# Kernel tuning notes

Hardware: AMD Instinct MI355X
Metric: run time of the kernel (lower is better)

## Reference

```python
import jax, jax.numpy as jnp
import numpy as np

B, T, C, H = 2, 2048, 1024, 16
HD = C // H          # head dim = 64
HD2 = HD // 2        # rotary half = 32


def setup_inputs() -> dict:
    key = jax.random.key(0)
    k0, k1, k2 = jax.random.split(key, 3)
    x = jax.random.normal(k0, (B, T, C), jnp.float32)
    Wqkv = jax.random.normal(k1, (C, 3 * C), jnp.float32) * (1.0 / np.sqrt(C))
    bqkv = jnp.zeros((3 * C,), jnp.float32)
    Wproj = jax.random.normal(k2, (C, C), jnp.float32) * (1.0 / np.sqrt(C))
    bproj = jnp.zeros((C,), jnp.float32)
    # standard rotary frequencies: theta_i = 10000^{-2i/hd}
    inv_freq = 1.0 / (10000.0 ** (jnp.arange(0, HD, 2, dtype=jnp.float32) / HD))
    angles = jnp.arange(T, dtype=jnp.float32)[:, None] * inv_freq[None, :]  # (T, HD2)
    return {
        "x": x,
        "freqs_cos": jnp.cos(angles),
        "freqs_sin": jnp.sin(angles),
        "Wqkv": Wqkv,
        "bqkv": bqkv,
        "Wproj": Wproj,
        "bproj": bproj,
    }


def _rope(u, cos, sin):
    # u: (B, T, H, HD); half-split pairing: (u[i], u[i + HD/2]) form a complex pair
    u1, u2 = u[..., :HD2], u[..., HD2:]
    c = cos[None, :, None, :]  # (1, T, 1, HD2)
    s = sin[None, :, None, :]
    return jnp.concatenate([u1 * c - u2 * s, u1 * s + u2 * c], axis=-1)


def reference(x, freqs_cos, freqs_sin, Wqkv, bqkv, Wproj, bproj):
    Bc, Tc, Cc = x.shape
    qkv = x @ Wqkv + bqkv                      # (B, T, 3C)
    q, k, v = jnp.split(qkv, 3, axis=-1)
    q = q.reshape(Bc, Tc, H, HD)
    k = k.reshape(Bc, Tc, H, HD)
    v = v.reshape(Bc, Tc, H, HD)
    q = _rope(q, freqs_cos, freqs_sin)
    k = _rope(k, freqs_cos, freqs_sin)
    scale = 1.0 / np.sqrt(HD)
    scores = jnp.einsum("bthd,bshd->bhts", q, k) * scale  # (B, H, T, T)
    causal = jnp.tril(jnp.ones((Tc, Tc), dtype=bool))
    scores = jnp.where(causal[None, None], scores, jnp.finfo(scores.dtype).min)
    p = jax.nn.softmax(scores, axis=-1)
    y = jnp.einsum("bhts,bshd->bthd", p, v).reshape(Bc, Tc, Cc)
    return y @ Wproj + bproj
```

## Files before the change

kernel.cpp:

```cpp
#include <hip/hip_runtime.h>
#include <hip/hip_bf16.h>
#include <cstdint>
#include <cmath>

typedef __bf16 bf16_t;
typedef __attribute__((ext_vector_type(8))) __bf16 bf16x8;
typedef __attribute__((ext_vector_type(4))) float f32x4;

#define LOG2E 1.4426950408889634f

constexpr int B_ = 2, T_ = 2048, C_ = 1024, H_ = 16, HD_ = 64, HD2_ = 32;
constexpr int M_ = B_ * T_;

static __device__ __forceinline__ f32x4 mfma16(bf16x8 a, bf16x8 b, f32x4 c) {
    return __builtin_amdgcn_mfma_f32_16x16x32_bf16(a, b, c, 0, 0, 0);
}

#define GLL(gp, lp)                                                          \
    __builtin_amdgcn_global_load_lds(                                        \
        (const __attribute__((address_space(1))) void*)(gp),                 \
        (__attribute__((address_space(3))) void*)(lp), 16, 0, 0)

__global__ void prep(const float* __restrict__ x, bf16_t* __restrict__ xb,
                     const float* __restrict__ Wqkv, bf16_t* __restrict__ wqkvT,
                     const float* __restrict__ Wproj, bf16_t* __restrict__ wprojT) {
    __shared__ float tile[32][33];
    const int bid = blockIdx.x, tid = threadIdx.x;
    if (bid < 4096) {
        int i = bid * 256 + tid;
        float4 v = ((const float4*)x)[i];
        bf16_t o[4] = {(bf16_t)v.x, (bf16_t)v.y, (bf16_t)v.z, (bf16_t)v.w};
        *(uint64_t*)(xb + (size_t)i * 4) = *(uint64_t*)o;
        return;
    }
    const float* W;
    bf16_t* WT;
    int K, N, nb, kb;
    if (bid < 4096 + 3072) {
        int t = bid - 4096;
        W = Wqkv; WT = wqkvT; K = C_; N = 3 * C_;
        nb = (t % 96) * 32; kb = (t / 96) * 32;
    } else {
        int t = bid - 7168;
        W = Wproj; WT = wprojT; K = C_; N = C_;
        nb = (t & 31) * 32; kb = (t >> 5) * 32;
    }
    int tx = tid & 31, ty = tid >> 5;
    for (int i = ty; i < 32; i += 8)
        tile[i][tx] = W[(size_t)(kb + i) * N + nb + tx];
    __syncthreads();
    for (int i = ty; i < 32; i += 8)
        WT[(size_t)(nb + i) * K + kb + tx] = (bf16_t)tile[tx][i];
}

template <int MODE>
__global__ __launch_bounds__(256, 3) void gemm128(
    const bf16_t* __restrict__ A, const bf16_t* __restrict__ BT, const float* __restrict__ bias,
    int N, int K,
    bf16_t* __restrict__ Qb, bf16_t* __restrict__ Kb, bf16_t* __restrict__ VTb,
    const float* __restrict__ cosT, const float* __restrict__ sinT, float* __restrict__ out) {
    constexpr int NT = (MODE == 1) ? 2 : 4;
    constexpr int BPARTS = (MODE == 1) ? 2 : 4;
    __shared__ alignas(16) bf16_t As[128 * 64];
    __shared__ alignas(16) bf16_t Bs[32 * BPARTS * 64];
    const int tid = threadIdx.x;
    const int w = tid >> 6, lane = tid & 63;
    const int quad = lane >> 4, r = lane & 15;
    const int wm = (w >> 1) * 64, wn = (w & 1) * (16 * NT);
    const int bid = blockIdx.x;
    const int xcd = bid & 7, s = bid >> 3;
    int mb, nb;
    if (MODE == 0) {
        mb = (((xcd >> 1) << 3) + (s & 7)) << 7;
        nb = (((xcd & 1) * 12 + (s >> 3))) << 7;
    } else {
        mb = (((xcd >> 1) << 3) + (s & 7)) << 7;
        nb = (((xcd & 1) << 3) + (s >> 3)) << 6;
    }
    const int srow = tid >> 3, schunk = tid & 7;
    const int csw = (schunk ^ (srow & 7)) * 8;
    const int koff0 = (quad ^ (r & 7)) * 8;
    const int koff1 = ((quad + 4) ^ (r & 7)) * 8;

    f32x4 acc[4][NT] = {};

    const bf16_t* gA[4];
    const bf16_t* gB[BPARTS];
#pragma unroll
    for (int p = 0; p < 4; p++) gA[p] = A + (size_t)(mb + p * 32 + srow) * K + csw;
#pragma unroll
    for (int p = 0; p < BPARTS; p++) gB[p] = BT + (size_t)(nb + p * 32 + srow) * K + csw;

    for (int k0 = 0; k0 < K; k0 += 64) {
        __syncthreads();
#pragma unroll
        for (int p = 0; p < 4; p++) GLL(gA[p] + k0, As + p * 2048 + tid * 8);
#pragma unroll
        for (int p = 0; p < BPARTS; p++) GLL(gB[p] + k0, Bs + p * 2048 + tid * 8);
        __syncthreads();
#pragma unroll
        for (int h = 0; h < 2; h++) {
            const int ko = h ? koff1 : koff0;
            bf16x8 af[4], bfr[NT];
#pragma unroll
            for (int i = 0; i < 4; i++) af[i] = *(const bf16x8*)(As + (wm + i * 16 + r) * 64 + ko);
#pragma unroll
            for (int j = 0; j < NT; j++) bfr[j] = *(const bf16x8*)(Bs + (wn + j * 16 + r) * 64 + ko);
#pragma unroll
            for (int i = 0; i < 4; i++)
#pragma unroll
                for (int j = 0; j < NT; j++) acc[i][j] = mfma16(af[i], bfr[j], acc[i][j]);
        }
    }

    if (MODE == 0) {
        const int col_base = nb + wn;
        const int region = col_base >> 10;
        const int h = (col_base & 1023) >> 6;
        const float qscale = 0.125f * LOG2E;
        if (region < 2) {
#pragma unroll
            for (int i = 0; i < 4; i++) {
#pragma unroll
                for (int g = 0; g < 4; g++) {
                    int m = mb + wm + i * 16 + quad * 4 + g;
                    int b = m >> 11, t = m & (T_ - 1);
                    bf16_t* dst = (region == 0 ? Qb : Kb) + ((size_t)((b * H_ + h) * T_ + t)) * 64;
                    int tw = t & 7;
#pragma unroll
                    for (int j = 0; j < 2; j++) {
                        int d = j * 16 + r;
                        float u1 = acc[i][j][g] + bias[col_base + d];
                        float u2 = acc[i][j + 2][g] + bias[col_base + d + 32];
                        float c = cosT[t * HD2_ + d], s2 = sinT[t * HD2_ + d];
                        float o1 = u1 * c - u2 * s2;
                        float o2 = u1 * s2 + u2 * c;
                        if (region == 0) {
                            dst[d] = (bf16_t)(o1 * qscale);
                            dst[d + 32] = (bf16_t)(o2 * qscale);
                        } else {
                            dst[((((d >> 3) ^ tw)) << 3) | (d & 7)] = (bf16_t)o1;
                            dst[(((((d + 32) >> 3) ^ tw)) << 3) | (d & 7)] = (bf16_t)o2;
                        }
                    }
                }
            }
        } else {
#pragma unroll
            for (int i = 0; i < 4; i++) {
                int m0 = mb + wm + i * 16 + quad * 4;
                int b = m0 >> 11, t0 = m0 & (T_ - 1);
                bf16_t* base = VTb + (size_t)(b * H_ + h) * 64 * T_;
#pragma unroll
                for (int j = 0; j < 4; j++) {
                    int d = j * 16 + r;
                    float bb = bias[col_base + d];
                    bf16_t pk[4];
#pragma unroll
                    for (int g = 0; g < 4; g++) pk[g] = (bf16_t)(acc[i][j][g] + bb);
                    int c = (((t0 >> 3) & 7) ^ (d & 7));
                    int tsw = (t0 & ~63) | (c << 3) | (t0 & 7);
                    *(uint64_t*)(base + (size_t)d * T_ + tsw) = *(uint64_t*)pk;
                }
            }
        }
    } else {
#pragma unroll
        for (int i = 0; i < 4; i++)
#pragma unroll
            for (int g = 0; g < 4; g++) {
                int m = mb + wm + i * 16 + quad * 4 + g;
#pragma unroll
                for (int j = 0; j < NT; j++) {
                    int col = nb + wn + j * 16 + r;
                    out[(size_t)m * N + col] = acc[i][j][g] + bias[col];
                }
            }
    }
}

__global__ __launch_bounds__(512, 4) void attn64(
    const bf16_t* __restrict__ Qb, const bf16_t* __restrict__ Kb,
    const bf16_t* __restrict__ VTb, bf16_t* __restrict__ att) {
    __shared__ alignas(16) bf16_t Ks[2][2][4096];
    __shared__ alignas(16) bf16_t Vs[2][2][4096];
    __shared__ alignas(16) bf16_t Ps[8][1024];
    const int tid = threadIdx.x;
    const int w = tid >> 6, lane = tid & 63;
    const int grp = w >> 2, wq = w & 3;
    const int quad = lane >> 4, r = lane & 15;
    const int id = blockIdx.x;
    const int t = 31 - (id >> 5);
    const int bh = id & 31;
    const int ntiles = t + 1, nstages = (t + 2) >> 1;
    const size_t kbase = (size_t)bh * T_ * 64;
    const size_t vbase = (size_t)bh * 64 * T_;
    bf16_t* Pw = &Ps[w][0];
    const int srow = tid >> 3, schunk = tid & 7;
    const int koff0 = ((quad ^ (r & 7)) * 8);
    const int koff1 = (((quad + 4) ^ (r & 7)) * 8);

    const int qrow = t * 64 + wq * 16 + r;
    bf16x8 qf0 = *(const bf16x8*)(Qb + kbase + (size_t)qrow * 64 + quad * 8);
    bf16x8 qf1 = *(const bf16x8*)(Qb + kbase + (size_t)qrow * 64 + 32 + quad * 8);

    f32x4 oacc[4] = {};
    float l = 0.f;

    {
        const bf16_t* kg = Kb + kbase + (size_t)srow * 64 + schunk * 8;
        GLL(kg, &Ks[0][0][0] + tid * 8);
        const bf16_t* vg = VTb + vbase + (size_t)srow * T_ + schunk * 8;
        GLL(vg, &Vs[0][0][0] + tid * 8);
        if (1 < ntiles) {
            GLL(kg + 64 * 64, &Ks[0][1][0] + tid * 8);
            GLL(vg + 64, &Vs[0][1][0] + tid * 8);
        }
    }
    for (int s = 0; s < nstages; s++) {
        const int cur = s & 1;
        __syncthreads();
        if (s + 1 < nstages) {
            const int ja = 2 * (s + 1);
            const bf16_t* kg = Kb + kbase + (size_t)(ja * 64 + srow) * 64 + schunk * 8;
            const bf16_t* vg = VTb + vbase + (size_t)srow * T_ + ja * 64 + schunk * 8;
            GLL(kg, &Ks[cur ^ 1][0][0] + tid * 8);
            GLL(vg, &Vs[cur ^ 1][0][0] + tid * 8);
            if (ja + 1 < ntiles) {
                GLL(kg + 64 * 64, &Ks[cur ^ 1][1][0] + tid * 8);
                GLL(vg + 64, &Vs[cur ^ 1][1][0] + tid * 8);
            }
        }
        const int jt = 2 * s + grp;
        if (jt < ntiles) {
            const bf16_t* Kt = &Ks[cur][grp][0];
            const bf16_t* Vt = &Vs[cur][grp][0];
            f32x4 sc[4];
#pragma unroll
            for (int m0 = 0; m0 < 4; m0++) {
                const bf16_t* kp = Kt + (m0 * 16 + r) * 64;
                bf16x8 kf0 = *(const bf16x8*)(kp + koff0);
                bf16x8 kf1 = *(const bf16x8*)(kp + koff1);
                f32x4 z = {0.f, 0.f, 0.f, 0.f};
                z = mfma16(kf0, qf0, z);
                z = mfma16(kf1, qf1, z);
                sc[m0] = z;
            }
            if (jt == t) {
                const int j0 = jt * 64;
#pragma unroll
                for (int m0 = 0; m0 < 4; m0++) {
                    int kvb = j0 + m0 * 16 + quad * 4;
#pragma unroll
                    for (int g = 0; g < 4; g++)
                        if (kvb + g > qrow) sc[m0][g] = -INFINITY;
                }
            }
            float rs = 0.f;
#pragma unroll
            for (int m0 = 0; m0 < 4; m0++)
#pragma unroll
                for (int g = 0; g < 4; g++) {
                    float pp = __builtin_amdgcn_exp2f(sc[m0][g]);
                    sc[m0][g] = pp;
                    rs += pp;
                }
            l += rs;
#pragma unroll
            for (int m0 = 0; m0 < 4; m0++) {
                bf16_t hq[4];
#pragma unroll
                for (int g = 0; g < 4; g++) hq[g] = (bf16_t)sc[m0][g];
                int elem = (m0 >> 1) * 512 + (((m0 & 1) * 2 + (quad >> 1)) * 16 + r) * 8 + (quad & 1) * 4;
                *(uint64_t*)(Pw + elem) = *(uint64_t*)hq;
            }
            __builtin_amdgcn_wave_barrier();
            bf16x8 pf0 = *(const bf16x8*)(Pw + lane * 8);
            bf16x8 pf1 = *(const bf16x8*)(Pw + 512 + lane * 8);
#pragma unroll
            for (int d0 = 0; d0 < 4; d0++) {
                const bf16_t* vp = Vt + (d0 * 16 + r) * 64;
                bf16x8 vf0 = *(const bf16x8*)(vp + koff0);
                bf16x8 vf1 = *(const bf16x8*)(vp + koff1);
                oacc[d0] = mfma16(vf0, pf0, oacc[d0]);
                oacc[d0] = mfma16(vf1, pf1, oacc[d0]);
            }
        }
    }
    l += __shfl_xor(l, 16);
    l += __shfl_xor(l, 32);
    __syncthreads();
    float* Co = (float*)&Ks[0][0][0];
    float* Cl = (float*)&Vs[0][0][0];
    if (grp == 1) {
#pragma unroll
        for (int d0 = 0; d0 < 4; d0++)
            *(f32x4*)(Co + wq * 1024 + r * 64 + d0 * 16 + quad * 4) = oacc[d0];
        if (quad == 0) Cl[wq * 16 + r] = l;
    }
    __syncthreads();
    if (grp == 0) {
        float inv = 1.f / (l + Cl[wq * 16 + r]);
        const int b = bh >> 4, h = bh & 15;
        bf16_t* dst = att + ((size_t)(b * T_ + qrow)) * 1024 + h * 64;
#pragma unroll
        for (int d0 = 0; d0 < 4; d0++) {
            f32x4 o1 = *(const f32x4*)(Co + wq * 1024 + r * 64 + d0 * 16 + quad * 4);
            bf16_t hh[4];
#pragma unroll
            for (int g = 0; g < 4; g++)
                hh[g] = (bf16_t)((oacc[d0][g] + o1[g]) * inv);
            *(uint64_t*)(dst + d0 * 16 + quad * 4) = *(uint64_t*)hh;
        }
    }
}

extern "C" void kernel_launch(void* const* d_in, const int* in_sizes, int n_in,
                              void* d_out, int out_size, void* d_ws, size_t ws_size,
                              hipStream_t stream) {
    const float* x = (const float*)d_in[0];
    const float* fcos = (const float*)d_in[1];
    const float* fsin = (const float*)d_in[2];
    const float* Wqkv = (const float*)d_in[3];
    const float* bqkv = (const float*)d_in[4];
    const float* Wproj = (const float*)d_in[5];
    const float* bproj = (const float*)d_in[6];
    float* out = (float*)d_out;

    uint8_t* p = (uint8_t*)d_ws;
    size_t need = 0;
    auto take = [&](size_t bytes) {
        void* q = p;
        size_t pad = (bytes + 255) & ~(size_t)255;
        p += pad;
        need += pad;
        return q;
    };
    bf16_t* xb = (bf16_t*)take((size_t)M_ * C_ * 2);
    bf16_t* wqkvT = (bf16_t*)take((size_t)3 * C_ * C_ * 2);
    bf16_t* wprojT = (bf16_t*)take((size_t)C_ * C_ * 2);
    bf16_t* Qb = (bf16_t*)take((size_t)B_ * H_ * T_ * 64 * 2);
    bf16_t* Kb = (bf16_t*)take((size_t)B_ * H_ * T_ * 64 * 2);
    bf16_t* VTb = (bf16_t*)take((size_t)B_ * H_ * 64 * T_ * 2);
    bf16_t* attb = (bf16_t*)take((size_t)M_ * C_ * 2);
    if (ws_size < need) return;

    prep<<<8192, 256, 0, stream>>>(x, xb, Wqkv, wqkvT, Wproj, wprojT);

    gemm128<0><<<dim3(768), 256, 0, stream>>>(
        xb, wqkvT, bqkv, 3 * C_, C_, Qb, Kb, VTb, fcos, fsin, nullptr);

    attn64<<<dim3(1024), 512, 0, stream>>>(Qb, Kb, VTb, attb);

    gemm128<1><<<dim3(512), 256, 0, stream>>>(
        attb, wprojT, bproj, C_, C_, nullptr, nullptr, nullptr, nullptr, nullptr, out);
}
```

Before: 174.8 us.

## Load V fragments directly to registers and vectorize weight transpose prep

The attention kernel no longer stages V tiles through shared memory. Each wave loads its V fragments straight from global memory into registers at the start of each stage, while K double-buffering stays in LDS with clamped tile indices. This cuts LDS use, which allows a higher occupancy hint (launch_bounds 6), at the cost of less-coalesced global V reads whose latency has to be hidden behind the QK computation. The prep kernel is also vectorized: 8 elements per thread for the x cast, and 64x32 transpose tiles with 16-byte bf16 stores, halving the block count.

```diff
diff --git a/kernel.cpp b/kernel.cpp
--- a/kernel.cpp
+++ b/kernel.cpp
@@ -24,33 +24,48 @@
 __global__ void prep(const float* __restrict__ x, bf16_t* __restrict__ xb,
                      const float* __restrict__ Wqkv, bf16_t* __restrict__ wqkvT,
                      const float* __restrict__ Wproj, bf16_t* __restrict__ wprojT) {
-    __shared__ float tile[32][33];
     const int bid = blockIdx.x, tid = threadIdx.x;
-    if (bid < 4096) {
-        int i = bid * 256 + tid;
-        float4 v = ((const float4*)x)[i];
-        bf16_t o[4] = {(bf16_t)v.x, (bf16_t)v.y, (bf16_t)v.z, (bf16_t)v.w};
-        *(uint64_t*)(xb + (size_t)i * 4) = *(uint64_t*)o;
+    if (bid < 2048) {
+        size_t i = ((size_t)bid * 256 + tid) * 8;
+        float4 v0 = *(const float4*)(x + i);
+        float4 v1 = *(const float4*)(x + i + 4);
+        union { bf16_t h[8]; uint4 u; } pk;
+        pk.h[0] = (bf16_t)v0.x; pk.h[1] = (bf16_t)v0.y;
+        pk.h[2] = (bf16_t)v0.z; pk.h[3] = (bf16_t)v0.w;
+        pk.h[4] = (bf16_t)v1.x; pk.h[5] = (bf16_t)v1.y;
+        pk.h[6] = (bf16_t)v1.z; pk.h[7] = (bf16_t)v1.w;
+        *(uint4*)(xb + i) = pk.u;
         return;
     }
+    __shared__ float tile[32][66];
     const float* W;
     bf16_t* WT;
-    int K, N, nb, kb;
-    if (bid < 4096 + 3072) {
-        int t = bid - 4096;
-        W = Wqkv; WT = wqkvT; K = C_; N = 3 * C_;
-        nb = (t % 96) * 32; kb = (t / 96) * 32;
+    int N, nb, kb;
+    if (bid < 3584) {
+        int t = bid - 2048;
+        W = Wqkv; WT = wqkvT; N = 3 * C_;
+        nb = (t % 48) * 64; kb = (t / 48) * 32;
     } else {
-        int t = bid - 7168;
-        W = Wproj; WT = wprojT; K = C_; N = C_;
-        nb = (t & 31) * 32; kb = (t >> 5) * 32;
-    }
-    int tx = tid & 31, ty = tid >> 5;
-    for (int i = ty; i < 32; i += 8)
-        tile[i][tx] = W[(size_t)(kb + i) * N + nb + tx];
+        int t = bid - 3584;
+        W = Wproj; WT = wprojT; N = C_;
+        nb = (t & 15) * 64; kb = (t >> 4) * 32;
+    }
+    const int row = tid >> 3, colg = (tid & 7) * 8;
+    {
+        const float* src = W + (size_t)(kb + row) * N + nb + colg;
+        float4 a = *(const float4*)src;
+        float4 b = *(const float4*)(src + 4);
+        *(float2*)&tile[row][colg] = make_float2(a.x, a.y);
+        *(float2*)&tile[row][colg + 2] = make_float2(a.z, a.w);
+        *(float2*)&tile[row][colg + 4] = make_float2(b.x, b.y);
+        *(float2*)&tile[row][colg + 6] = make_float2(b.z, b.w);
+    }
     __syncthreads();
-    for (int i = ty; i < 32; i += 8)
-        WT[(size_t)(nb + i) * K + kb + tx] = (bf16_t)tile[tx][i];
+    const int n = tid >> 2, kg = (tid & 3) * 8;
+    union { bf16_t h[8]; uint4 u; } pk;
+#pragma unroll
+    for (int j = 0; j < 8; j++) pk.h[j] = (bf16_t)tile[kg + j][n];
+    *(uint4*)(WT + (size_t)(nb + n) * C_ + kb + kg) = pk.u;
 }
 
 template <int MODE>
@@ -179,11 +194,10 @@
     }
 }
 
-__global__ __launch_bounds__(512, 4) void attn64(
+__global__ __launch_bounds__(512, 6) void attn64(
     const bf16_t* __restrict__ Qb, const bf16_t* __restrict__ Kb,
     const bf16_t* __restrict__ VTb, bf16_t* __restrict__ att) {
     __shared__ alignas(16) bf16_t Ks[2][2][4096];
-    __shared__ alignas(16) bf16_t Vs[2][2][4096];
     __shared__ alignas(16) bf16_t Ps[8][1024];
     const int tid = threadIdx.x;
     const int w = tid >> 6, lane = tid & 63;
@@ -207,34 +221,32 @@
     f32x4 oacc[4] = {};
     float l = 0.f;
 
-    {
-        const bf16_t* kg = Kb + kbase + (size_t)srow * 64 + schunk * 8;
-        GLL(kg, &Ks[0][0][0] + tid * 8);
-        const bf16_t* vg = VTb + vbase + (size_t)srow * T_ + schunk * 8;
-        GLL(vg, &Vs[0][0][0] + tid * 8);
-        if (1 < ntiles) {
-            GLL(kg + 64 * 64, &Ks[0][1][0] + tid * 8);
-            GLL(vg + 64, &Vs[0][1][0] + tid * 8);
-        }
-    }
+    auto stageK = [&](int jt0, int jt1, int buf) {
+        GLL(Kb + kbase + (size_t)(jt0 * 64 + srow) * 64 + schunk * 8, &Ks[buf][0][0] + tid * 8);
+        GLL(Kb + kbase + (size_t)(jt1 * 64 + srow) * 64 + schunk * 8, &Ks[buf][1][0] + tid * 8);
+    };
+    stageK(0, min(1, t), 0);
     for (int s = 0; s < nstages; s++) {
         const int cur = s & 1;
+        const int jt = 2 * s + grp;
+        const int jtc = min(jt, t);
         __syncthreads();
-        if (s + 1 < nstages) {
+        bf16x8 vf[4][2];
+        {
+            const bf16_t* vrow = VTb + vbase + (size_t)r * T_ + jtc * 64;
+#pragma unroll
+            for (int d0 = 0; d0 < 4; d0++) {
+                const bf16_t* vp = vrow + (size_t)(d0 * 16) * T_;
+                vf[d0][0] = *(const bf16x8*)(vp + koff0);
+                vf[d0][1] = *(const bf16x8*)(vp + koff1);
+            }
+        }
+        {
             const int ja = 2 * (s + 1);
-            const bf16_t* kg = Kb + kbase + (size_t)(ja * 64 + srow) * 64 + schunk * 8;
-            const bf16_t* vg = VTb + vbase + (size_t)srow * T_ + ja * 64 + schunk * 8;
-            GLL(kg, &Ks[cur ^ 1][0][0] + tid * 8);
-            GLL(vg, &Vs[cur ^ 1][0][0] + tid * 8);
-            if (ja + 1 < ntiles) {
-                GLL(kg + 64 * 64, &Ks[cur ^ 1][1][0] + tid * 8);
-                GLL(vg + 64, &Vs[cur ^ 1][1][0] + tid * 8);
-            }
-        }
-        const int jt = 2 * s + grp;
+            stageK(min(ja, t), min(ja + 1, t), cur ^ 1);
+        }
         if (jt < ntiles) {
             const bf16_t* Kt = &Ks[cur][grp][0];
-            const bf16_t* Vt = &Vs[cur][grp][0];
             f32x4 sc[4];
 #pragma unroll
             for (int m0 = 0; m0 < 4; m0++) {
@@ -279,11 +291,8 @@
             bf16x8 pf1 = *(const bf16x8*)(Pw + 512 + lane * 8);
 #pragma unroll
             for (int d0 = 0; d0 < 4; d0++) {
-                const bf16_t* vp = Vt + (d0 * 16 + r) * 64;
-                bf16x8 vf0 = *(const bf16x8*)(vp + koff0);
-                bf16x8 vf1 = *(const bf16x8*)(vp + koff1);
-                oacc[d0] = mfma16(vf0, pf0, oacc[d0]);
-                oacc[d0] = mfma16(vf1, pf1, oacc[d0]);
+                oacc[d0] = mfma16(vf[d0][0], pf0, oacc[d0]);
+                oacc[d0] = mfma16(vf[d0][1], pf1, oacc[d0]);
             }
         }
     }
@@ -291,7 +300,7 @@
     l += __shfl_xor(l, 32);
     __syncthreads();
     float* Co = (float*)&Ks[0][0][0];
-    float* Cl = (float*)&Vs[0][0][0];
+    float* Cl = Co + 4096;
     if (grp == 1) {
 #pragma unroll
         for (int d0 = 0; d0 < 4; d0++)
@@ -345,7 +354,7 @@
     bf16_t* attb = (bf16_t*)take((size_t)M_ * C_ * 2);
     if (ws_size < need) return;
 
-    prep<<<8192, 256, 0, stream>>>(x, xb, Wqkv, wqkvT, Wproj, wprojT);
+    prep<<<4096, 256, 0, stream>>>(x, xb, Wqkv, wqkvT, Wproj, wprojT);
 
     gemm128<0><<<dim3(768), 256, 0, stream>>>(
         xb, wqkvT, bqkv, 3 * C_, C_, Qb, Kb, VTb, fcos, fsin, nullptr);
```

After: 235.5 us. 1.35x slower.
